# Performance work log

Measured on AMD Instinct MI355X. Metric: run time of the kernel, lower is better.

The kernel has to match this reference:

```python
import jax, jax.numpy as jnp
import numpy as np


def setup_inputs() -> dict:
    key = jax.random.key(0)
    kq, kk, kv = jax.random.split(key, 3)
    B, HQ, HKV, S, D = 1, 32, 8, 2048, 128
    return {
        "query": jax.random.normal(kq, (B, HQ, S, D), dtype=jnp.float32),
        "key": jax.random.normal(kk, (B, HKV, S, D), dtype=jnp.float32),
        "value": jax.random.normal(kv, (B, HKV, S, D), dtype=jnp.float32),
    }


def reference(query, key, value):
    # RawSDP.forward with is_causal=True, attn_mask=None, dropout_p=0, scale=None
    b, hq, sq, d = query.shape
    hkv = key.shape[1]
    reps = hq // hkv  # GQA group size
    # repeak_kv: expand each kv head `reps` times contiguously along head axis
    key = jnp.repeat(key, reps, axis=1)    # [b, hq, skv, d]
    value = jnp.repeat(value, reps, axis=1)
    skv = key.shape[2]
    half_sqrt = 1.0 / jnp.sqrt(jnp.sqrt(jnp.float32(d)))  # scale split across q and k
    scores = jnp.einsum("bhqd,bhkd->bhqk", query * half_sqrt, key * half_sqrt)
    # causal tril bool mask -> additive mask (0 where allowed, finfo.min where not)
    causal = jnp.tril(jnp.ones((sq, skv), dtype=bool))
    neg = jnp.finfo(query.dtype).min
    scores = scores + jnp.where(causal, jnp.zeros((), query.dtype), neg)
    # softmax computed in float32, cast back to query dtype
    attn = jax.nn.softmax(scores.astype(jnp.float32), axis=-1).astype(query.dtype)
    return jnp.einsum("bhqk,bhkd->bhqd", attn, value)
```

## Files before the change

kernel.cpp:

```cpp
#include <hip/hip_runtime.h>
#include <hip/hip_bf16.h>
#include <stdint.h>

typedef __attribute__((ext_vector_type(8))) short bf16x8;
typedef __attribute__((ext_vector_type(4))) float f32x4;
typedef __attribute__((ext_vector_type(16))) float f32x16;

#define S_LEN 2048
#define D_DIM 128
#define HQ_N  32
#define KVB   32
#define NT    64
#define KTILE_B 8192
#define VTILE_B 8192

__device__ __forceinline__ ushort f2bf(float f) {
  union { float f; uint32_t u; } c; c.f = f;
  uint32_t u = c.u;
  u += 0x7FFFu + ((u >> 16) & 1u);
  return (ushort)(u >> 16);
}

__device__ __forceinline__ uint32_t cvtpk(float lo, float hi) {
  uint32_t r;
  asm("v_cvt_pk_bf16_f32 %0, %1, %2" : "=v"(r) : "v"(lo), "v"(hi));
  return r;
}

__device__ __forceinline__ float xhalf_max(float x) {
  uint32_t a = __builtin_bit_cast(uint32_t, x), b;
  asm volatile("v_mov_b32 %0, %1" : "=&v"(b) : "v"(a));
  asm volatile("v_permlane32_swap_b32 %0, %1" : "+v"(a), "+v"(b));
  return fmaxf(__builtin_bit_cast(float, a), __builtin_bit_cast(float, b));
}

__global__ __launch_bounds__(256) void prep_k(const float* __restrict__ K,
                                              ushort* __restrict__ KT) {
  int tid  = blockIdx.x * 256 + threadIdx.x;
  int tile = tid >> 9;
  int c    = tid & 511;
  int s    = c >> 6;
  int lane = c & 63;
  int l31  = lane & 31, hi = lane >> 5;
  const float* src = K + ((size_t)(tile * 32 + l31)) * D_DIM + 16 * s + 8 * hi;
  float4 x = *(const float4*)src;
  float4 y = *(const float4*)(src + 4);
  union { ushort u[8]; bf16x8 v; } o;
  o.u[0] = f2bf(x.x); o.u[1] = f2bf(x.y); o.u[2] = f2bf(x.z); o.u[3] = f2bf(x.w);
  o.u[4] = f2bf(y.x); o.u[5] = f2bf(y.y); o.u[6] = f2bf(y.z); o.u[7] = f2bf(y.w);
  *(bf16x8*)(KT + (size_t)tid * 8) = o.v;
}

__global__ __launch_bounds__(256) void prep_v(const float* __restrict__ V,
                                              ushort* __restrict__ VT) {
  int tid  = blockIdx.x * 256 + threadIdx.x;
  int tile = tid >> 9;
  int cc   = tid & 511;
  int l31  = cc & 31;
  int hi   = (cc >> 5) & 1;
  int c    = (cc >> 6) & 1;
  int dt   = cc >> 7;
  int hkv  = tile >> 6, kt = tile & 63;
  const float* src = V + ((size_t)hkv * S_LEN + kt * 32 + 16 * c + 8 * hi) * D_DIM
                       + 32 * dt + l31;
  union { ushort u[8]; bf16x8 v; } o;
  #pragma unroll
  for (int jj = 0; jj < 8; ++jj) o.u[jj] = f2bf(src[(size_t)jj * D_DIM]);
  *(bf16x8*)(VT + (size_t)tid * 8) = o.v;
}

__device__ __forceinline__ void step32(
    int kt, int j, int qrow, int hi, int lane,
    const char* kt_base, const char* vt_base,
    const bf16x8 (&qf)[8], bf16x8 (&KC)[8], bf16x8 (&KN)[8],
    const bf16x8& ones, const f32x16& zero16,
    f32x16 (&o4)[4], float& mrow, float& lsum) {
  bf16x8 vf[8];
  const char* vp = vt_base + (size_t)kt * VTILE_B;
  #pragma unroll
  for (int u = 0; u < 8; ++u)
    vf[u] = *(const bf16x8*)(vp + (u * 64 + lane) * 16);
  if (kt < j) {
    const char* kp2 = kt_base + (size_t)(kt + 1) * KTILE_B;
    #pragma unroll
    for (int s = 0; s < 8; ++s)
      KN[s] = *(const bf16x8*)(kp2 + (s * 64 + lane) * 16);
  }

  f32x16 st = {};
  __builtin_amdgcn_s_setprio(1);
  #pragma unroll
  for (int s = 0; s < 8; ++s)
    st = __builtin_amdgcn_mfma_f32_32x32x16_bf16(KC[s], qf[s], st, 0, 0, 0);
  __builtin_amdgcn_s_setprio(0);

  if (kt == j) {
    #pragma unroll
    for (int r = 0; r < 16; ++r) {
      int kv = KVB * kt + (r & 3) + 8 * (r >> 2) + 4 * hi;
      if (kv > qrow) st[r] = -1e30f;
    }
  }

  float t8[8];
  #pragma unroll
  for (int e = 0; e < 8; ++e) t8[e] = fmaxf(st[e], st[e + 8]);
  float mx = fmaxf(fmaxf(fmaxf(t8[0], t8[1]), fmaxf(t8[2], t8[3])),
                   fmaxf(fmaxf(t8[4], t8[5]), fmaxf(t8[6], t8[7])));
  mx = xhalf_max(mx);
  if (!__all(mx <= mrow + 8.0f)) {
    float mnew = fmaxf(mrow, mx);
    float alpha = exp2f(mrow - mnew);
    #pragma unroll
    for (int dt = 0; dt < 4; ++dt) o4[dt] *= alpha;
    lsum *= alpha;
    mrow = mnew;
  }

  #pragma unroll
  for (int e = 0; e < 16; ++e) st[e] = exp2f(st[e] - mrow);

  bf16x8 pb[2];
  #pragma unroll
  for (int c = 0; c < 2; ++c) {
    const int r0 = c * 8;
    uint32_t a0 = cvtpk(st[r0 + 0], st[r0 + 1]);
    uint32_t b0 = cvtpk(st[r0 + 4], st[r0 + 5]);
    asm volatile("v_permlane32_swap_b32 %0, %1" : "+v"(a0), "+v"(b0));
    uint32_t a1 = cvtpk(st[r0 + 2], st[r0 + 3]);
    uint32_t b1 = cvtpk(st[r0 + 6], st[r0 + 7]);
    asm volatile("v_permlane32_swap_b32 %0, %1" : "+v"(a1), "+v"(b1));
    union { uint32_t u[4]; bf16x8 v; } pu;
    pu.u[0] = a0; pu.u[1] = a1; pu.u[2] = b0; pu.u[3] = b1;
    pb[c] = pu.v;
  }

  f32x16 pbsum = __builtin_amdgcn_mfma_f32_32x32x16_bf16(ones, pb[0], zero16, 0, 0, 0);
  pbsum = __builtin_amdgcn_mfma_f32_32x32x16_bf16(ones, pb[1], pbsum, 0, 0, 0);

  __builtin_amdgcn_s_setprio(1);
  #pragma unroll
  for (int dt = 0; dt < 4; ++dt) {
    o4[dt] = __builtin_amdgcn_mfma_f32_32x32x16_bf16(vf[2 * dt + 0], pb[0], o4[dt], 0, 0, 0);
    o4[dt] = __builtin_amdgcn_mfma_f32_32x32x16_bf16(vf[2 * dt + 1], pb[1], o4[dt], 0, 0, 0);
  }
  __builtin_amdgcn_s_setprio(0);

  lsum += pbsum[0];
}

__global__ __launch_bounds__(64, 2) void attn_fwd(
    const float* __restrict__ Q, const ushort* __restrict__ KT,
    const ushort* __restrict__ VT, float* __restrict__ O) {
  const int id   = blockIdx.x;
  const int g    = id & 7;
  const int rest = id >> 3;
  const int qh   = rest & 3;
  const int j    = 63 - (rest >> 2);
  const int h    = g * 4 + qh;
  const int lane = threadIdx.x;
  const int l31  = lane & 31;
  const int hi   = lane >> 5;
  const int qrow = j * 32 + l31;

  const char* kt_base = (const char*)KT + (size_t)g * NT * KTILE_B;
  const char* vt_base = (const char*)VT + (size_t)g * NT * VTILE_B;

  const float scale = 0.08838834764831845f * 1.4426950408889634f;
  bf16x8 qf[8];
  {
    const float* qp = Q + ((size_t)h * S_LEN + qrow) * D_DIM;
    #pragma unroll
    for (int s = 0; s < 8; ++s) {
      const float* p = qp + 16 * s + 8 * hi;
      float4 x = *(const float4*)p;
      float4 y = *(const float4*)(p + 4);
      bf16x8 f;
      f[0] = (short)f2bf(x.x * scale); f[1] = (short)f2bf(x.y * scale);
      f[2] = (short)f2bf(x.z * scale); f[3] = (short)f2bf(x.w * scale);
      f[4] = (short)f2bf(y.x * scale); f[5] = (short)f2bf(y.y * scale);
      f[6] = (short)f2bf(y.z * scale); f[7] = (short)f2bf(y.w * scale);
      qf[s] = f;
    }
  }

  bf16x8 ones;
  #pragma unroll
  for (int s = 0; s < 8; ++s) ones[s] = (short)0x3F80;
  const f32x16 zero16 = {};

  f32x16 o4[4] = {};
  float mrow = -1e30f, lsum = 0.f;

  bf16x8 kfa[8], kfb[8];
  #pragma unroll
  for (int s = 0; s < 8; ++s)
    kfa[s] = *(const bf16x8*)(kt_base + (s * 64 + lane) * 16);

  int kt = 0;
  for (;;) {
    step32(kt, j, qrow, hi, lane, kt_base, vt_base, qf, kfa, kfb, ones, zero16,
           o4, mrow, lsum);
    if (++kt > j) break;
    step32(kt, j, qrow, hi, lane, kt_base, vt_base, qf, kfb, kfa, ones, zero16,
           o4, mrow, lsum);
    if (++kt > j) break;
  }

  const float inv = 1.0f / lsum;
  float* op = O + ((size_t)h * S_LEN + qrow) * D_DIM;
  #pragma unroll
  for (int dt = 0; dt < 4; ++dt)
    #pragma unroll
    for (int rq = 0; rq < 4; ++rq) {
      f32x4 vv;
      #pragma unroll
      for (int jj = 0; jj < 4; ++jj) vv[jj] = o4[dt][rq * 4 + jj] * inv;
      *(f32x4*)(op + 32 * dt + 8 * rq + 4 * hi) = vv;
    }
}

extern "C" void kernel_launch(void* const* d_in, const int* in_sizes, int n_in,
                              void* d_out, int out_size, void* d_ws, size_t ws_size,
                              hipStream_t stream) {
  const float* Q = (const float*)d_in[0];
  const float* K = (const float*)d_in[1];
  const float* V = (const float*)d_in[2];
  float* O = (float*)d_out;
  ushort* wsK = (ushort*)d_ws;
  ushort* wsV = wsK + (size_t)8 * NT * (KTILE_B / 2);
  prep_k<<<1024, 256, 0, stream>>>(K, wsK);
  prep_v<<<1024, 256, 0, stream>>>(V, wsV);
  attn_fwd<<<2048, 64, 0, stream>>>(Q, wsK, wsV, O);
}
```

Before: 82.43 us.

## Process 64-key blocks per iteration, dropping K double-buffer prefetch

```diff
diff --git a/kernel.cpp b/kernel.cpp
--- a/kernel.cpp
+++ b/kernel.cpp
@@ -9,10 +9,8 @@
 #define S_LEN 2048
 #define D_DIM 128
 #define HQ_N  32
-#define KVB   32
-#define NT    64
-#define KTILE_B 8192
-#define VTILE_B 8192
+#define NT32  64
+#define SUB_B 8192
 
 __device__ __forceinline__ ushort f2bf(float f) {
   union { float f; uint32_t u; } c; c.f = f;
@@ -60,93 +58,13 @@
   int hi   = (cc >> 5) & 1;
   int c    = (cc >> 6) & 1;
   int dt   = cc >> 7;
-  int hkv  = tile >> 6, kt = tile & 63;
-  const float* src = V + ((size_t)hkv * S_LEN + kt * 32 + 16 * c + 8 * hi) * D_DIM
+  int hkv  = tile >> 6, ktv = tile & 63;
+  const float* src = V + ((size_t)hkv * S_LEN + ktv * 32 + 16 * c + 8 * hi) * D_DIM
                        + 32 * dt + l31;
   union { ushort u[8]; bf16x8 v; } o;
   #pragma unroll
   for (int jj = 0; jj < 8; ++jj) o.u[jj] = f2bf(src[(size_t)jj * D_DIM]);
   *(bf16x8*)(VT + (size_t)tid * 8) = o.v;
-}
-
-__device__ __forceinline__ void step32(
-    int kt, int j, int qrow, int hi, int lane,
-    const char* kt_base, const char* vt_base,
-    const bf16x8 (&qf)[8], bf16x8 (&KC)[8], bf16x8 (&KN)[8],
-    const bf16x8& ones, const f32x16& zero16,
-    f32x16 (&o4)[4], float& mrow, float& lsum) {
-  bf16x8 vf[8];
-  const char* vp = vt_base + (size_t)kt * VTILE_B;
-  #pragma unroll
-  for (int u = 0; u < 8; ++u)
-    vf[u] = *(const bf16x8*)(vp + (u * 64 + lane) * 16);
-  if (kt < j) {
-    const char* kp2 = kt_base + (size_t)(kt + 1) * KTILE_B;
-    #pragma unroll
-    for (int s = 0; s < 8; ++s)
-      KN[s] = *(const bf16x8*)(kp2 + (s * 64 + lane) * 16);
-  }
-
-  f32x16 st = {};
-  __builtin_amdgcn_s_setprio(1);
-  #pragma unroll
-  for (int s = 0; s < 8; ++s)
-    st = __builtin_amdgcn_mfma_f32_32x32x16_bf16(KC[s], qf[s], st, 0, 0, 0);
-  __builtin_amdgcn_s_setprio(0);
-
-  if (kt == j) {
-    #pragma unroll
-    for (int r = 0; r < 16; ++r) {
-      int kv = KVB * kt + (r & 3) + 8 * (r >> 2) + 4 * hi;
-      if (kv > qrow) st[r] = -1e30f;
-    }
-  }
-
-  float t8[8];
-  #pragma unroll
-  for (int e = 0; e < 8; ++e) t8[e] = fmaxf(st[e], st[e + 8]);
-  float mx = fmaxf(fmaxf(fmaxf(t8[0], t8[1]), fmaxf(t8[2], t8[3])),
-                   fmaxf(fmaxf(t8[4], t8[5]), fmaxf(t8[6], t8[7])));
-  mx = xhalf_max(mx);
-  if (!__all(mx <= mrow + 8.0f)) {
-    float mnew = fmaxf(mrow, mx);
-    float alpha = exp2f(mrow - mnew);
-    #pragma unroll
-    for (int dt = 0; dt < 4; ++dt) o4[dt] *= alpha;
-    lsum *= alpha;
-    mrow = mnew;
-  }
-
-  #pragma unroll
-  for (int e = 0; e < 16; ++e) st[e] = exp2f(st[e] - mrow);
-
-  bf16x8 pb[2];
-  #pragma unroll
-  for (int c = 0; c < 2; ++c) {
-    const int r0 = c * 8;
-    uint32_t a0 = cvtpk(st[r0 + 0], st[r0 + 1]);
-    uint32_t b0 = cvtpk(st[r0 + 4], st[r0 + 5]);
-    asm volatile("v_permlane32_swap_b32 %0, %1" : "+v"(a0), "+v"(b0));
-    uint32_t a1 = cvtpk(st[r0 + 2], st[r0 + 3]);
-    uint32_t b1 = cvtpk(st[r0 + 6], st[r0 + 7]);
-    asm volatile("v_permlane32_swap_b32 %0, %1" : "+v"(a1), "+v"(b1));
-    union { uint32_t u[4]; bf16x8 v; } pu;
-    pu.u[0] = a0; pu.u[1] = a1; pu.u[2] = b0; pu.u[3] = b1;
-    pb[c] = pu.v;
-  }
-
-  f32x16 pbsum = __builtin_amdgcn_mfma_f32_32x32x16_bf16(ones, pb[0], zero16, 0, 0, 0);
-  pbsum = __builtin_amdgcn_mfma_f32_32x32x16_bf16(ones, pb[1], pbsum, 0, 0, 0);
-
-  __builtin_amdgcn_s_setprio(1);
-  #pragma unroll
-  for (int dt = 0; dt < 4; ++dt) {
-    o4[dt] = __builtin_amdgcn_mfma_f32_32x32x16_bf16(vf[2 * dt + 0], pb[0], o4[dt], 0, 0, 0);
-    o4[dt] = __builtin_amdgcn_mfma_f32_32x32x16_bf16(vf[2 * dt + 1], pb[1], o4[dt], 0, 0, 0);
-  }
-  __builtin_amdgcn_s_setprio(0);
-
-  lsum += pbsum[0];
 }
 
 __global__ __launch_bounds__(64, 2) void attn_fwd(
@@ -162,9 +80,10 @@
   const int l31  = lane & 31;
   const int hi   = lane >> 5;
   const int qrow = j * 32 + l31;
-
-  const char* kt_base = (const char*)KT + (size_t)g * NT * KTILE_B;
-  const char* vt_base = (const char*)VT + (size_t)g * NT * VTILE_B;
+  const int jt   = j >> 1;
+
+  const char* kt_base = (const char*)KT + (size_t)g * NT32 * SUB_B;
+  const char* vt_base = (const char*)VT + (size_t)g * NT32 * SUB_B;
 
   const float scale = 0.08838834764831845f * 1.4426950408889634f;
   bf16x8 qf[8];
@@ -192,19 +111,101 @@
   f32x16 o4[4] = {};
   float mrow = -1e30f, lsum = 0.f;
 
-  bf16x8 kfa[8], kfb[8];
-  #pragma unroll
-  for (int s = 0; s < 8; ++s)
-    kfa[s] = *(const bf16x8*)(kt_base + (s * 64 + lane) * 16);
-
-  int kt = 0;
-  for (;;) {
-    step32(kt, j, qrow, hi, lane, kt_base, vt_base, qf, kfa, kfb, ones, zero16,
-           o4, mrow, lsum);
-    if (++kt > j) break;
-    step32(kt, j, qrow, hi, lane, kt_base, vt_base, qf, kfb, kfa, ones, zero16,
-           o4, mrow, lsum);
-    if (++kt > j) break;
+  for (int kt = 0; kt <= jt; ++kt) {
+    const char* kp = kt_base + (size_t)kt * (2 * SUB_B);
+
+    bf16x8 kf[16];
+    #pragma unroll
+    for (int t = 0; t < 2; ++t)
+      #pragma unroll
+      for (int s = 0; s < 8; ++s)
+        kf[t * 8 + s] = *(const bf16x8*)(kp + t * SUB_B + (s * 64 + lane) * 16);
+    bf16x8 vfA[8], vfB[8];
+    const char* vp = vt_base + (size_t)(2 * kt) * SUB_B;
+    #pragma unroll
+    for (int ks = 0; ks < 2; ++ks)
+      #pragma unroll
+      for (int dt = 0; dt < 4; ++dt)
+        vfA[ks * 4 + dt] = *(const bf16x8*)(vp + (dt * 128 + ks * 64 + lane) * 16);
+
+    f32x16 st[2] = {};
+    __builtin_amdgcn_s_setprio(1);
+    #pragma unroll
+    for (int t = 0; t < 2; ++t)
+      #pragma unroll
+      for (int s = 0; s < 8; ++s)
+        st[t] = __builtin_amdgcn_mfma_f32_32x32x16_bf16(kf[t * 8 + s], qf[s], st[t], 0, 0, 0);
+    __builtin_amdgcn_s_setprio(0);
+
+    #pragma unroll
+    for (int ks = 0; ks < 2; ++ks)
+      #pragma unroll
+      for (int dt = 0; dt < 4; ++dt)
+        vfB[ks * 4 + dt] = *(const bf16x8*)(vp + SUB_B + (dt * 128 + ks * 64 + lane) * 16);
+
+    if (kt == jt) {
+      #pragma unroll
+      for (int t = 0; t < 2; ++t)
+        #pragma unroll
+        for (int r = 0; r < 16; ++r) {
+          int kv = 64 * kt + 32 * t + (r & 3) + 8 * (r >> 2) + 4 * hi;
+          if (kv > qrow) st[t][r] = -1e30f;
+        }
+    }
+
+    float t16[8];
+    #pragma unroll
+    for (int e = 0; e < 8; ++e)
+      t16[e] = fmaxf(fmaxf(st[0][e], st[0][e + 8]), fmaxf(st[1][e], st[1][e + 8]));
+    float mx = fmaxf(fmaxf(fmaxf(t16[0], t16[1]), fmaxf(t16[2], t16[3])),
+                     fmaxf(fmaxf(t16[4], t16[5]), fmaxf(t16[6], t16[7])));
+    mx = xhalf_max(mx);
+    if (!__all(mx <= mrow + 8.0f)) {
+      float mnew = fmaxf(mrow, mx);
+      float alpha = exp2f(mrow - mnew);
+      #pragma unroll
+      for (int dt = 0; dt < 4; ++dt) o4[dt] *= alpha;
+      lsum *= alpha;
+      mrow = mnew;
+    }
+    #pragma unroll
+    for (int t = 0; t < 2; ++t)
+      #pragma unroll
+      for (int e = 0; e < 16; ++e) st[t][e] = exp2f(st[t][e] - mrow);
+
+    bf16x8 pb[4];
+    #pragma unroll
+    for (int t = 0; t < 2; ++t)
+      #pragma unroll
+      for (int c = 0; c < 2; ++c) {
+        const int r0 = c * 8;
+        uint32_t a0 = cvtpk(st[t][r0 + 0], st[t][r0 + 1]);
+        uint32_t b0 = cvtpk(st[t][r0 + 4], st[t][r0 + 5]);
+        asm volatile("v_permlane32_swap_b32 %0, %1" : "+v"(a0), "+v"(b0));
+        uint32_t a1 = cvtpk(st[t][r0 + 2], st[t][r0 + 3]);
+        uint32_t b1 = cvtpk(st[t][r0 + 6], st[t][r0 + 7]);
+        asm volatile("v_permlane32_swap_b32 %0, %1" : "+v"(a1), "+v"(b1));
+        union { uint32_t u[4]; bf16x8 v; } pu;
+        pu.u[0] = a0; pu.u[1] = a1; pu.u[2] = b0; pu.u[3] = b1;
+        pb[t * 2 + c] = pu.v;
+      }
+
+    f32x16 pbsum = __builtin_amdgcn_mfma_f32_32x32x16_bf16(ones, pb[0], zero16, 0, 0, 0);
+    pbsum = __builtin_amdgcn_mfma_f32_32x32x16_bf16(ones, pb[1], pbsum, 0, 0, 0);
+    pbsum = __builtin_amdgcn_mfma_f32_32x32x16_bf16(ones, pb[2], pbsum, 0, 0, 0);
+    pbsum = __builtin_amdgcn_mfma_f32_32x32x16_bf16(ones, pb[3], pbsum, 0, 0, 0);
+
+    __builtin_amdgcn_s_setprio(1);
+    #pragma unroll
+    for (int dt = 0; dt < 4; ++dt) {
+      o4[dt] = __builtin_amdgcn_mfma_f32_32x32x16_bf16(vfA[0 * 4 + dt], pb[0], o4[dt], 0, 0, 0);
+      o4[dt] = __builtin_amdgcn_mfma_f32_32x32x16_bf16(vfA[1 * 4 + dt], pb[1], o4[dt], 0, 0, 0);
+      o4[dt] = __builtin_amdgcn_mfma_f32_32x32x16_bf16(vfB[0 * 4 + dt], pb[2], o4[dt], 0, 0, 0);
+      o4[dt] = __builtin_amdgcn_mfma_f32_32x32x16_bf16(vfB[1 * 4 + dt], pb[3], o4[dt], 0, 0, 0);
+    }
+    __builtin_amdgcn_s_setprio(0);
+
+    lsum += pbsum[0];
   }
 
   const float inv = 1.0f / lsum;
@@ -228,7 +229,7 @@
   const float* V = (const float*)d_in[2];
   float* O = (float*)d_out;
   ushort* wsK = (ushort*)d_ws;
-  ushort* wsV = wsK + (size_t)8 * NT * (KTILE_B / 2);
+  ushort* wsV = wsK + (size_t)8 * NT32 * (SUB_B / 2);
   prep_k<<<1024, 256, 0, stream>>>(K, wsK);
   prep_v<<<1024, 256, 0, stream>>>(V, wsV);
   attn_fwd<<<2048, 64, 0, stream>>>(Q, wsK, wsV, O);
```

Measured after the change: 82.42 us. About the same (-0.0%).

## Double-buffer V tiles in registers and interleave heavy/light causal blocks

Applied to the files above, without the earlier changes.

```diff
diff --git a/kernel.cpp b/kernel.cpp
--- a/kernel.cpp
+++ b/kernel.cpp
@@ -9,10 +9,8 @@
 #define S_LEN 2048
 #define D_DIM 128
 #define HQ_N  32
-#define KVB   32
-#define NT    64
-#define KTILE_B 8192
-#define VTILE_B 8192
+#define NT32  64
+#define SUB_B 8192
 
 __device__ __forceinline__ ushort f2bf(float f) {
   union { float f; uint32_t u; } c; c.f = f;
@@ -60,8 +58,8 @@
   int hi   = (cc >> 5) & 1;
   int c    = (cc >> 6) & 1;
   int dt   = cc >> 7;
-  int hkv  = tile >> 6, kt = tile & 63;
-  const float* src = V + ((size_t)hkv * S_LEN + kt * 32 + 16 * c + 8 * hi) * D_DIM
+  int hkv  = tile >> 6, ktv = tile & 63;
+  const float* src = V + ((size_t)hkv * S_LEN + ktv * 32 + 16 * c + 8 * hi) * D_DIM
                        + 32 * dt + l31;
   union { ushort u[8]; bf16x8 v; } o;
   #pragma unroll
@@ -69,23 +67,21 @@
   *(bf16x8*)(VT + (size_t)tid * 8) = o.v;
 }
 
-__device__ __forceinline__ void step32(
+__device__ __forceinline__ void step_pipe(
     int kt, int j, int qrow, int hi, int lane,
     const char* kt_base, const char* vt_base,
-    const bf16x8 (&qf)[8], bf16x8 (&KC)[8], bf16x8 (&KN)[8],
+    const bf16x8 (&qf)[8],
+    bf16x8 (&KC)[8], bf16x8 (&VC)[8],
+    bf16x8 (&KN)[8], bf16x8 (&VN)[8],
     const bf16x8& ones, const f32x16& zero16,
     f32x16 (&o4)[4], float& mrow, float& lsum) {
-  bf16x8 vf[8];
-  const char* vp = vt_base + (size_t)kt * VTILE_B;
-  #pragma unroll
-  for (int u = 0; u < 8; ++u)
-    vf[u] = *(const bf16x8*)(vp + (u * 64 + lane) * 16);
   if (kt < j) {
-    const char* kp2 = kt_base + (size_t)(kt + 1) * KTILE_B;
+    const char* kp2 = kt_base + (size_t)(kt + 1) * SUB_B;
     #pragma unroll
     for (int s = 0; s < 8; ++s)
       KN[s] = *(const bf16x8*)(kp2 + (s * 64 + lane) * 16);
   }
+  __builtin_amdgcn_sched_barrier(0);
 
   f32x16 st = {};
   __builtin_amdgcn_s_setprio(1);
@@ -93,11 +89,20 @@
   for (int s = 0; s < 8; ++s)
     st = __builtin_amdgcn_mfma_f32_32x32x16_bf16(KC[s], qf[s], st, 0, 0, 0);
   __builtin_amdgcn_s_setprio(0);
+  __builtin_amdgcn_sched_barrier(0);
+
+  if (kt < j) {
+    const char* vp2 = vt_base + (size_t)(kt + 1) * SUB_B;
+    #pragma unroll
+    for (int u = 0; u < 8; ++u)
+      VN[u] = *(const bf16x8*)(vp2 + (u * 64 + lane) * 16);
+  }
+  __builtin_amdgcn_sched_barrier(0);
 
   if (kt == j) {
     #pragma unroll
     for (int r = 0; r < 16; ++r) {
-      int kv = KVB * kt + (r & 3) + 8 * (r >> 2) + 4 * hi;
+      int kv = 32 * kt + (r & 3) + 8 * (r >> 2) + 4 * hi;
       if (kv > qrow) st[r] = -1e30f;
     }
   }
@@ -116,7 +121,6 @@
     lsum *= alpha;
     mrow = mnew;
   }
-
   #pragma unroll
   for (int e = 0; e < 16; ++e) st[e] = exp2f(st[e] - mrow);
 
@@ -137,15 +141,13 @@
 
   f32x16 pbsum = __builtin_amdgcn_mfma_f32_32x32x16_bf16(ones, pb[0], zero16, 0, 0, 0);
   pbsum = __builtin_amdgcn_mfma_f32_32x32x16_bf16(ones, pb[1], pbsum, 0, 0, 0);
-
   __builtin_amdgcn_s_setprio(1);
   #pragma unroll
   for (int dt = 0; dt < 4; ++dt) {
-    o4[dt] = __builtin_amdgcn_mfma_f32_32x32x16_bf16(vf[2 * dt + 0], pb[0], o4[dt], 0, 0, 0);
-    o4[dt] = __builtin_amdgcn_mfma_f32_32x32x16_bf16(vf[2 * dt + 1], pb[1], o4[dt], 0, 0, 0);
+    o4[dt] = __builtin_amdgcn_mfma_f32_32x32x16_bf16(VC[2 * dt + 0], pb[0], o4[dt], 0, 0, 0);
+    o4[dt] = __builtin_amdgcn_mfma_f32_32x32x16_bf16(VC[2 * dt + 1], pb[1], o4[dt], 0, 0, 0);
   }
   __builtin_amdgcn_s_setprio(0);
-
   lsum += pbsum[0];
 }
 
@@ -154,17 +156,18 @@
     const ushort* __restrict__ VT, float* __restrict__ O) {
   const int id   = blockIdx.x;
   const int g    = id & 7;
-  const int rest = id >> 3;
-  const int qh   = rest & 3;
-  const int j    = 63 - (rest >> 2);
+  const int c    = (id >> 3) & 31;
+  const int qh   = (id >> 8) & 3;
+  const int p    = (id >> 10) & 1;
+  const int j    = p ? (63 - c) : c;
   const int h    = g * 4 + qh;
   const int lane = threadIdx.x;
   const int l31  = lane & 31;
   const int hi   = lane >> 5;
   const int qrow = j * 32 + l31;
 
-  const char* kt_base = (const char*)KT + (size_t)g * NT * KTILE_B;
-  const char* vt_base = (const char*)VT + (size_t)g * NT * VTILE_B;
+  const char* kt_base = (const char*)KT + (size_t)g * NT32 * SUB_B;
+  const char* vt_base = (const char*)VT + (size_t)g * NT32 * SUB_B;
 
   const float scale = 0.08838834764831845f * 1.4426950408889634f;
   bf16x8 qf[8];
@@ -172,9 +175,9 @@
     const float* qp = Q + ((size_t)h * S_LEN + qrow) * D_DIM;
     #pragma unroll
     for (int s = 0; s < 8; ++s) {
-      const float* p = qp + 16 * s + 8 * hi;
-      float4 x = *(const float4*)p;
-      float4 y = *(const float4*)(p + 4);
+      const float* px = qp + 16 * s + 8 * hi;
+      float4 x = *(const float4*)px;
+      float4 y = *(const float4*)(px + 4);
       bf16x8 f;
       f[0] = (short)f2bf(x.x * scale); f[1] = (short)f2bf(x.y * scale);
       f[2] = (short)f2bf(x.z * scale); f[3] = (short)f2bf(x.w * scale);
@@ -192,18 +195,21 @@
   f32x16 o4[4] = {};
   float mrow = -1e30f, lsum = 0.f;
 
-  bf16x8 kfa[8], kfb[8];
+  bf16x8 KA[8], VA[8], KB[8], VB[8];
   #pragma unroll
   for (int s = 0; s < 8; ++s)
-    kfa[s] = *(const bf16x8*)(kt_base + (s * 64 + lane) * 16);
+    KA[s] = *(const bf16x8*)(kt_base + (s * 64 + lane) * 16);
+  #pragma unroll
+  for (int u = 0; u < 8; ++u)
+    VA[u] = *(const bf16x8*)(vt_base + (u * 64 + lane) * 16);
 
   int kt = 0;
   for (;;) {
-    step32(kt, j, qrow, hi, lane, kt_base, vt_base, qf, kfa, kfb, ones, zero16,
-           o4, mrow, lsum);
+    step_pipe(kt, j, qrow, hi, lane, kt_base, vt_base, qf, KA, VA, KB, VB,
+              ones, zero16, o4, mrow, lsum);
     if (++kt > j) break;
-    step32(kt, j, qrow, hi, lane, kt_base, vt_base, qf, kfb, kfa, ones, zero16,
-           o4, mrow, lsum);
+    step_pipe(kt, j, qrow, hi, lane, kt_base, vt_base, qf, KB, VB, KA, VA,
+              ones, zero16, o4, mrow, lsum);
     if (++kt > j) break;
   }
 
@@ -228,7 +234,7 @@
   const float* V = (const float*)d_in[2];
   float* O = (float*)d_out;
   ushort* wsK = (ushort*)d_ws;
-  ushort* wsV = wsK + (size_t)8 * NT * (KTILE_B / 2);
+  ushort* wsV = wsK + (size_t)8 * NT32 * (SUB_B / 2);
   prep_k<<<1024, 256, 0, stream>>>(K, wsK);
   prep_v<<<1024, 256, 0, stream>>>(V, wsV);
   attn_fwd<<<2048, 64, 0, stream>>>(Q, wsK, wsV, O);
```

New measurement: 89.32 us. +8.4%, slower.
